# Kernel optimization log

Hardware: AMD Instinct MI355X
Metric: run time of the kernel (lower is better)

Reference implementation:

```python
import jax, jax.numpy as jnp
import numpy as np

B, H, W, K, P = 2, 1080, 1920, 2048, 256
MAX_R = 6  # max box radius -> (R+1) averaged maps, 13x13 max kernel


def _kernel_bank():
    coords = np.arange(-MAX_R, MAX_R + 1, dtype=np.float32)
    gy, gx = np.meshgrid(coords, coords, indexing='ij')
    r = np.arange(MAX_R + 1, dtype=np.float32)[:, None, None]
    mask = ((np.abs(gy) <= r) & (np.abs(gx) <= r)).astype(np.float32)
    denom = np.maximum((2.0 * r + 1.0) ** 2, 1.0)
    return jnp.asarray((mask / denom)[:, None])  # (R+1, 1, k, k) OIHW

KERNEL = _kernel_bank()


def setup_inputs() -> dict:
    key = jax.random.key(0)
    ks = jax.random.split(key, 9)
    image = jax.random.normal(ks[0], (B, 1, H, W), jnp.float32)
    keypoints = jax.random.uniform(ks[1], (B, K, 2), jnp.float32) * jnp.array([H - 1.0, W - 1.0], jnp.float32)
    orientation = (jax.random.uniform(ks[2], (B, 1, H, W), jnp.float32) * 2.0 - 1.0) * jnp.pi
    offset_y1 = jax.random.uniform(ks[3], (P,), jnp.float32) * 32.0 - 16.0
    offset_x1 = jax.random.uniform(ks[4], (P,), jnp.float32) * 32.0 - 16.0
    offset_y2 = jax.random.uniform(ks[5], (P,), jnp.float32) * 32.0 - 16.0
    offset_x2 = jax.random.uniform(ks[6], (P,), jnp.float32) * 32.0 - 16.0
    thresholds = jax.random.normal(ks[7], (P,), jnp.float32) * 0.1
    radii = jax.random.randint(ks[8], (P,), 0, MAX_R + 1, jnp.int32)
    return {"image": image, "keypoints": keypoints, "orientation": orientation,
            "offset_y1": offset_y1, "offset_x1": offset_x1,
            "offset_y2": offset_y2, "offset_x2": offset_x2,
            "thresholds": thresholds, "radii": radii}


def reference(image, keypoints, orientation, offset_y1, offset_x1, offset_y2, offset_x2, thresholds, radii):
    Bc, _, Hc, Wc = image.shape
    valid = (keypoints[..., 0] >= 0).astype(image.dtype)[..., None]  # (B,K,1)
    y = jnp.clip(keypoints[..., 0], 0.0, Hc - 1.0)
    x = jnp.clip(keypoints[..., 1], 0.0, Wc - 1.0)
    bidx = jnp.arange(Bc)[:, None]
    # grid_sample(orientation, nearest, border, align_corners=True) at keypoints
    iy = jnp.round(y).astype(jnp.int32)
    ix = jnp.round(x).astype(jnp.int32)
    theta = orientation[:, 0][bidx, iy, ix]  # (B,K)
    ct = jnp.cos(theta)[..., None]
    st = jnp.sin(theta)[..., None]
    oy1, ox1 = offset_y1[None, None], offset_x1[None, None]
    oy2, ox2 = offset_y2[None, None], offset_x2[None, None]
    rdy1 = ox1 * st + oy1 * ct
    rdx1 = ox1 * ct - oy1 * st
    rdy2 = ox2 * st + oy2 * ct
    rdx2 = ox2 * ct - oy2 * st
    p1y = y[..., None] + rdy1  # (B,K,P)
    p1x = x[..., None] + rdx1
    p2y = y[..., None] + rdy2
    p2x = x[..., None] + rdx2
    # box-averaged maps for every radius (depthwise-like conv bank)
    avg = jax.lax.conv_general_dilated(image, KERNEL.astype(image.dtype), (1, 1),
                                       [(MAX_R, MAX_R), (MAX_R, MAX_R)],
                                       dimension_numbers=('NCHW', 'OIHW', 'NCHW'))  # (B,R+1,H,W)
    avg_t = jnp.transpose(avg, (0, 2, 3, 1))  # (B,H,W,R+1)
    b3 = jnp.arange(Bc)[:, None, None]

    def samp(py, px):
        jy = jnp.clip(jnp.round(py), 0.0, Hc - 1.0).astype(jnp.int32)
        jx = jnp.clip(jnp.round(px), 0.0, Wc - 1.0).astype(jnp.int32)
        return avg_t[b3, jy, jx]  # (B,K,P,R+1)

    sel = jax.nn.one_hot(radii, MAX_R + 1, dtype=image.dtype)  # (P,R+1)
    v1 = jnp.einsum('bkpr,pr->bkp', samp(p1y, p1x), sel)
    v2 = jnp.einsum('bkpr,pr->bkp', samp(p2y, p2x), sel)
    desc = v1 - v2 - thresholds[None, None]  # binarize=False branch
    norm = jnp.linalg.norm(desc, axis=-1, keepdims=True)  # L2 normalize
    desc = desc / jnp.maximum(norm, 1e-12)
    return desc * valid
```

## Files before the change

kernel.cpp:

```cpp
#include <hip/hip_runtime.h>
#include <math.h>

#define B_ 2
#define H_ 1080
#define W_ 1920
#define K_ 2048
#define P_ 256

#define TW_ 61
#define SS_ 63
#define SATN_ ((TW_ + 1) * SS_)

__global__ __launch_bounds__(256) void bad_fused_kernel(
    const float* __restrict__ img, const float* __restrict__ kp,
    const float* __restrict__ orient,
    const float* __restrict__ oy1, const float* __restrict__ ox1,
    const float* __restrict__ oy2, const float* __restrict__ ox2,
    const float* __restrict__ thr, const int* __restrict__ radii,
    float* __restrict__ out) {
  __shared__ float S[SATN_];
  __shared__ float wsum[4];

  int tid = threadIdx.x;
  int lane = tid & 63;
  int wv = tid >> 6;
  int bk = blockIdx.x;
  int b = bk >> 11;

  float kpy = kp[(size_t)bk * 2 + 0];
  float kpx = kp[(size_t)bk * 2 + 1];
  float validf = (kpy >= 0.0f) ? 1.0f : 0.0f;
  float y = fminf(fmaxf(kpy, 0.0f), (float)(H_ - 1));
  float x = fminf(fmaxf(kpx, 0.0f), (float)(W_ - 1));
  int iy = (int)rintf(y);
  int ix = (int)rintf(x);
  float theta = orient[((size_t)b * H_ + iy) * W_ + ix];
  double td = (double)theta;
  float st = (float)sin(td);
  float ct = (float)cos(td);
  int ty0 = iy - 30, tx0 = ix - 30;
  const float* imgb = img + (size_t)b * H_ * W_;

  if (tid < SS_) S[tid] = 0.0f;
  if (tid < TW_ + 1) S[tid * SS_] = 0.0f;

  {
    int gx = tx0 + lane;
    bool cok = (lane < TW_) && (gx >= 0) && (gx < W_);
    for (int ly = wv; ly < TW_; ly += 4) {
      int gy = ty0 + ly;
      float v = 0.0f;
      if (cok && gy >= 0 && gy < H_) v = imgb[(size_t)gy * W_ + gx];
      if (lane < TW_) S[(ly + 1) * SS_ + lane + 1] = v;
    }
  }
  __syncthreads();

  if (tid < TW_) {
    float* Rw = S + (tid + 1) * SS_;
    double acc = 0.0;
    #pragma unroll 4
    for (int j = 1; j <= TW_; ++j) {
      acc += (double)Rw[j];
      Rw[j] = (float)acc;
    }
  }
  __syncthreads();

  if (tid < TW_) {
    float* Cw = S + (tid + 1);
    double acc = 0.0;
    #pragma unroll 4
    for (int j = 1; j <= TW_; ++j) {
      acc += (double)Cw[(size_t)j * SS_];
      Cw[(size_t)j * SS_] = (float)acc;
    }
  }
  __syncthreads();

  int p = tid;
  float a_y1 = oy1[p], a_x1 = ox1[p], a_y2 = oy2[p], a_x2 = ox2[p];
  float rdy1 = __fadd_rn(__fmul_rn(a_x1, st), __fmul_rn(a_y1, ct));
  float rdx1 = __fsub_rn(__fmul_rn(a_x1, ct), __fmul_rn(a_y1, st));
  float rdy2 = __fadd_rn(__fmul_rn(a_x2, st), __fmul_rn(a_y2, ct));
  float rdx2 = __fsub_rn(__fmul_rn(a_x2, ct), __fmul_rn(a_y2, st));
  float p1y = __fadd_rn(y, rdy1);
  float p1x = __fadd_rn(x, rdx1);
  float p2y = __fadd_rn(y, rdy2);
  float p2x = __fadd_rn(x, rdx2);

  int r = radii[p];
  float tt = 2.0f * (float)r + 1.0f;
  float w = __fdiv_rn(1.0f, __fmul_rn(tt, tt));

  int jy = (int)fminf(fmaxf(rintf(p1y), 0.0f), (float)(H_ - 1));
  int jx = (int)fminf(fmaxf(rintf(p1x), 0.0f), (float)(W_ - 1));
  int a0 = min(max(jy - r - ty0, 0), TW_);
  int a1 = min(max(jy + r - ty0 + 1, 0), TW_);
  int c0 = min(max(jx - r - tx0, 0), TW_);
  int c1 = min(max(jx + r - tx0 + 1, 0), TW_);
  float s1 = ((S[a1 * SS_ + c1] - S[a0 * SS_ + c1])
              - S[a1 * SS_ + c0]) + S[a0 * SS_ + c0];
  float v1 = __fmul_rn(s1, w);
  jy = (int)fminf(fmaxf(rintf(p2y), 0.0f), (float)(H_ - 1));
  jx = (int)fminf(fmaxf(rintf(p2x), 0.0f), (float)(W_ - 1));
  a0 = min(max(jy - r - ty0, 0), TW_);
  a1 = min(max(jy + r - ty0 + 1, 0), TW_);
  c0 = min(max(jx - r - tx0, 0), TW_);
  c1 = min(max(jx + r - tx0 + 1, 0), TW_);
  float s2 = ((S[a1 * SS_ + c1] - S[a0 * SS_ + c1])
              - S[a1 * SS_ + c0]) + S[a0 * SS_ + c0];
  float v2 = __fmul_rn(s2, w);

  float d = __fsub_rn(__fsub_rn(v1, v2), thr[p]);

  float sq = __fmul_rn(d, d);
  #pragma unroll
  for (int off = 32; off >= 1; off >>= 1) sq += __shfl_xor(sq, off, 64);
  if (lane == 0) wsum[wv] = sq;
  __syncthreads();
  float total = wsum[0] + wsum[1] + wsum[2] + wsum[3];
  float norm = sqrtf(total);
  float q = __fdiv_rn(d, fmaxf(norm, 1e-12f));
  out[(size_t)bk * P_ + p] = __fmul_rn(q, validf);
}


extern "C" void kernel_launch(void* const* d_in, const int* in_sizes, int n_in,
                              void* d_out, int out_size, void* d_ws, size_t ws_size,
                              hipStream_t stream) {
  const float* image    = (const float*)d_in[0];
  const float* kp       = (const float*)d_in[1];
  const float* orient   = (const float*)d_in[2];
  const float* oy1      = (const float*)d_in[3];
  const float* ox1      = (const float*)d_in[4];
  const float* oy2      = (const float*)d_in[5];
  const float* ox2      = (const float*)d_in[6];
  const float* thr      = (const float*)d_in[7];
  const int*   radii    = (const int*)d_in[8];
  float* out = (float*)d_out;

  bad_fused_kernel<<<B_ * K_, 256, 0, stream>>>(
      image, kp, orient, oy1, ox1, oy2, ox2, thr, radii, out);
}
```

Baseline: 116.6 us.

## Parallelize SAT prefix scans across 4 threads per row with shuffle combine

Splits each row and column prefix-sum of the 61x61 summed-area table into four 16-element segments handled by separate threads, combining segment totals with wave shuffles. Before, only 61 threads each did a serial 61-step scan. The tile load is also restructured to issue batches of 8 global loads before storing them, and the shared-memory stride is padded from 63 to 67 with extra zeroed rows so the segments stay in bounds. The cost is extra shuffle and partial-sum work, more padding to zero, and more shared memory; the padded stride may also change bank-conflict behaviour in the column pass.

```diff
diff --git a/kernel.cpp b/kernel.cpp
--- a/kernel.cpp
+++ b/kernel.cpp
@@ -8,8 +8,9 @@
 #define P_ 256
 
 #define TW_ 61
-#define SS_ 63
-#define SATN_ ((TW_ + 1) * SS_)
+#define SS_ 67
+#define NROWS_ 65
+#define SATN_ (NROWS_ * SS_ + 1)
 
 __global__ __launch_bounds__(256) void bad_fused_kernel(
     const float* __restrict__ img, const float* __restrict__ kp,
@@ -42,39 +43,68 @@
   const float* imgb = img + (size_t)b * H_ * W_;
 
   if (tid < SS_) S[tid] = 0.0f;
-  if (tid < TW_ + 1) S[tid * SS_] = 0.0f;
+  if (tid < 3 * SS_) S[62 * SS_ + tid] = 0.0f;
+  if (tid < TW_) S[(tid + 1) * SS_] = 0.0f;
+  if (tid == 0) S[SATN_ - 1] = 0.0f;
 
   {
     int gx = tx0 + lane;
     bool cok = (lane < TW_) && (gx >= 0) && (gx < W_);
-    for (int ly = wv; ly < TW_; ly += 4) {
-      int gy = ty0 + ly;
-      float v = 0.0f;
-      if (cok && gy >= 0 && gy < H_) v = imgb[(size_t)gy * W_ + gx];
-      if (lane < TW_) S[(ly + 1) * SS_ + lane + 1] = v;
+    #pragma unroll
+    for (int c = 0; c < 2; ++c) {
+      float v[8];
+      #pragma unroll
+      for (int k = 0; k < 8; ++k) {
+        int ly = wv + 4 * (8 * c + k);
+        int gy = ty0 + ly;
+        v[k] = 0.0f;
+        if (ly < TW_ && cok && gy >= 0 && gy < H_)
+          v[k] = imgb[(size_t)gy * W_ + gx];
+      }
+      #pragma unroll
+      for (int k = 0; k < 8; ++k) {
+        int ly = wv + 4 * (8 * c + k);
+        if (ly < TW_) S[(ly + 1) * SS_ + lane + 1] = v[k];
+      }
     }
   }
   __syncthreads();
 
-  if (tid < TW_) {
-    float* Rw = S + (tid + 1) * SS_;
+  if (tid < 244) {
+    int i = tid >> 2, s = tid & 3;
+    float* Rw = S + (i + 1) * SS_ + 16 * s + 1;
+    float v[16];
+    #pragma unroll
+    for (int k = 0; k < 16; ++k) v[k] = Rw[k];
     double acc = 0.0;
-    #pragma unroll 4
-    for (int j = 1; j <= TW_; ++j) {
-      acc += (double)Rw[j];
-      Rw[j] = (float)acc;
-    }
+    #pragma unroll
+    for (int k = 0; k < 16; ++k) acc += (double)v[k];
+    double inc = acc;
+    double n1 = __shfl_up(inc, 1, 64); if (s >= 1) inc += n1;
+    double n2 = __shfl_up(inc, 2, 64); if (s >= 2) inc += n2;
+    double e = __shfl_up(inc, 1, 64);
+    double a2 = (s >= 1) ? e : 0.0;
+    #pragma unroll
+    for (int k = 0; k < 16; ++k) { a2 += (double)v[k]; Rw[k] = (float)a2; }
   }
   __syncthreads();
 
-  if (tid < TW_) {
-    float* Cw = S + (tid + 1);
+  if (tid < 244) {
+    int i = tid >> 2, s = tid & 3;
+    float* Cw = S + (16 * s + 1) * SS_ + (i + 1);
+    float v[16];
+    #pragma unroll
+    for (int k = 0; k < 16; ++k) v[k] = Cw[k * SS_];
     double acc = 0.0;
-    #pragma unroll 4
-    for (int j = 1; j <= TW_; ++j) {
-      acc += (double)Cw[(size_t)j * SS_];
-      Cw[(size_t)j * SS_] = (float)acc;
-    }
+    #pragma unroll
+    for (int k = 0; k < 16; ++k) acc += (double)v[k];
+    double inc = acc;
+    double n1 = __shfl_up(inc, 1, 64); if (s >= 1) inc += n1;
+    double n2 = __shfl_up(inc, 2, 64); if (s >= 2) inc += n2;
+    double e = __shfl_up(inc, 1, 64);
+    double a2 = (s >= 1) ? e : 0.0;
+    #pragma unroll
+    for (int k = 0; k < 16; ++k) { a2 += (double)v[k]; Cw[k * SS_] = (float)a2; }
   }
   __syncthreads();
 
```

Result: faster. 108.1 us (-7.3%).
